# Optimization experiments

Hardware: AMD Instinct MI355X
Metric: run time of the kernel (lower is better)

## Reference

```python
import jax, jax.numpy as jnp
import numpy as np

NUM_GRAPHS = 256
N_NODES = 128          # nodes per graph (equal-size graphs)
DEG = 16               # average degree
NUM_EDGES = NUM_GRAPHS * N_NODES * DEG
NUM_HEADS = 8
SCALE = 10.0
INF_REPLACE = 1.0


def setup_inputs() -> dict:
    key = jax.random.key(0)
    k1, k2, k3 = jax.random.split(key, 3)
    # each graph owns a contiguous block of N_NODES global node ids
    eg = jnp.repeat(jnp.arange(NUM_GRAPHS, dtype=jnp.int32), N_NODES * DEG)
    src_loc = jax.random.randint(k1, (NUM_EDGES,), 0, N_NODES, dtype=jnp.int32)
    dst_loc = jax.random.randint(k2, (NUM_EDGES,), 0, N_NODES, dtype=jnp.int32)
    edge_index = jnp.stack([eg * N_NODES + src_loc, eg * N_NODES + dst_loc])  # [2, E]
    edge_weight = jax.random.uniform(k3, (NUM_EDGES,), minval=0.1, maxval=1.0)
    batch = jnp.repeat(jnp.arange(NUM_GRAPHS, dtype=jnp.int32), N_NODES)  # [N_total]
    return {
        'edge_index': edge_index,
        'edge_weight': edge_weight,
        'batch': batch,
        'num_graphs': NUM_GRAPHS,
        'max_num_nodes': N_NODES,
    }


def _shortest_path_bias(edge_index, edge_weight, batch, num_graphs, max_num_nodes):
    G, n = num_graphs, max_num_nodes
    inf = jnp.inf
    # per-graph node offsets (graphs occupy contiguous node-id blocks)
    counts = jnp.bincount(batch, length=G)
    offsets = jnp.concatenate([jnp.zeros((1,), counts.dtype), jnp.cumsum(counts)[:-1]])
    src, dst = edge_index[0], edge_index[1]
    eg = batch[src]                              # graph id of each edge
    u = src - offsets[eg]                        # local node ids
    v = dst - offsets[eg]
    # self-loops are skipped in the original (masked to +inf -> no-op under min)
    w = jnp.where(src == dst, inf, edge_weight)

    # init dense distance: inf off-diagonal, 0 on diagonal, edge weights scattered
    dist = jnp.full((G, n, n), inf, dtype=edge_weight.dtype)
    diag = jnp.arange(n)
    dist = dist.at[:, diag, diag].set(0.0)
    dist = dist.at[eg, u, v].min(w)

    # batched Floyd-Warshall: d[i,j] = min(d[i,j], d[i,k] + d[k,j]) for all graphs
    def body(d, k):
        col = jax.lax.dynamic_slice_in_dim(d, k, 1, axis=2)  # [G, n, 1] = d[:, :, k]
        row = jax.lax.dynamic_slice_in_dim(d, k, 1, axis=1)  # [G, 1, n] = d[:, k, :]
        return jnp.minimum(d, col + row), None
    dist, _ = jax.lax.scan(body, dist, jnp.arange(n))

    # replace unreachable with 2 * max finite distance (per graph)
    finite = jnp.isfinite(dist)
    fmax = jnp.max(jnp.where(finite, dist, -inf), axis=(1, 2), keepdims=True)
    unreach = jnp.where(jnp.isfinite(fmax), 2.0 * fmax, INF_REPLACE)
    dist = jnp.where(finite, dist, unreach)

    # normalize per graph and scale
    max_val = jnp.maximum(jnp.max(dist, axis=(1, 2), keepdims=True), 1e-8)
    bias = -SCALE * (dist / max_val)
    bias = jnp.nan_to_num(bias, nan=0.0, posinf=-1e6, neginf=-1e6)

    # expand over heads and flatten to [B*H, n, n]
    bias = jnp.broadcast_to(bias[:, None], (G, NUM_HEADS, n, n))
    return bias.reshape(G * NUM_HEADS, n, n)


def reference(edge_index, edge_weight, batch, num_graphs, max_num_nodes):
    return _shortest_path_bias(edge_index, edge_weight, batch, num_graphs, max_num_nodes)
```

## Files before the change

### kernel.cpp

```cpp
#include <hip/hip_runtime.h>

#define NHEADS 8
#define NN     128
#define NCELL  (NN * NN)
#define NT     512
#define SCALE_F 10.0f

typedef float nfloat4 __attribute__((ext_vector_type(4)));

#define RP_O 0
#define RP_N 2048
#define CP_As 4096
#define CP_Bs 6208
#define DPS  8320
#define RED  8640

template<int CBN>
__device__ __forceinline__ void extract_panels(const float (&dd)[4][8], float* lds,
                                               const int kbn, const int t,
                                               const int rgrp, const int cgrp,
                                               const int cpbase)
{
    if ((rgrp >> 2) == kbn) {
        const int q = rgrp & 3;
        #pragma unroll
        for (int rr = 0; rr < 4; ++rr) {
            const int iloc = 4 * q + rr;
            #pragma unroll
            for (int c = 0; c < 2; ++c) {
                *reinterpret_cast<float4*>(
                    &lds[RP_O + iloc * 128 + (cgrp << 2) + (c << 6)]) =
                    make_float4(dd[rr][c*4+0], dd[rr][c*4+1],
                                dd[rr][c*4+2], dd[rr][c*4+3]);
            }
        }
        const int p = cgrp - 4 * (kbn & 3);
        if ((unsigned)p < 4u) {
            #pragma unroll
            for (int rr = 0; rr < 4; ++rr) {
                *reinterpret_cast<float4*>(&lds[DPS + (4*q+rr) * 20 + (p << 2)]) =
                    make_float4(dd[rr][CBN+0], dd[rr][CBN+1],
                                dd[rr][CBN+2], dd[rr][CBN+3]);
            }
        }
    }
    {
        const int q2 = cgrp - 4 * (kbn & 3);
        if ((unsigned)q2 < 4u) {
            #pragma unroll
            for (int e = 0; e < 4; ++e) {
                const int m = 4 * q2 + e;
                *reinterpret_cast<float4*>(&lds[cpbase + m * 132 + (rgrp << 2)]) =
                    make_float4(dd[0][CBN+e], dd[1][CBN+e],
                                dd[2][CBN+e], dd[3][CBN+e]);
            }
        }
    }
}

__device__ __forceinline__ void closure(float* lds, const int t, const int kbn)
{
    if ((t >> 6) == kbn) {
        asm volatile("s_waitcnt lgkmcnt(0)" ::: "memory");
        const int l  = t & 63;
        const int i  = l & 15;
        const int jq = l >> 4;
        float4 v = *reinterpret_cast<const float4*>(&lds[DPS + i*20 + (jq << 2)]);
        float T0 = v.x, T1 = v.y, T2 = v.z, T3 = v.w;
        #pragma unroll
        for (int k = 0; k < 16; ++k) {
            const int ksrc = ((k >> 2) << 4) | i;
            float dik;
            switch (k & 3) {
                case 0: dik = __shfl(T0, ksrc); break;
                case 1: dik = __shfl(T1, ksrc); break;
                case 2: dik = __shfl(T2, ksrc); break;
                default: dik = __shfl(T3, ksrc); break;
            }
            const int rsrc = (jq << 4) | k;
            const float r0 = __shfl(T0, rsrc);
            const float r1 = __shfl(T1, rsrc);
            const float r2 = __shfl(T2, rsrc);
            const float r3 = __shfl(T3, rsrc);
            T0 = fminf(T0, dik + r0);
            T1 = fminf(T1, dik + r1);
            T2 = fminf(T2, dik + r2);
            T3 = fminf(T3, dik + r3);
        }
        *reinterpret_cast<float4*>(&lds[DPS + i*20 + (jq << 2)]) =
            make_float4(T0, T1, T2, T3);
    }
}

__device__ __forceinline__ void bprime(float* lds, const int t)
{
    const float INF = __builtin_huge_valf();
    const int r  = t >> 5;
    const int j4 = (t & 31) << 2;
    float da[16];
    #pragma unroll
    for (int q = 0; q < 4; ++q) {
        float4 d4 = *reinterpret_cast<const float4*>(&lds[DPS + r*20 + (q << 2)]);
        da[4*q+0]=d4.x; da[4*q+1]=d4.y; da[4*q+2]=d4.z; da[4*q+3]=d4.w;
    }
    float a0 = INF, a1 = INF, a2 = INF, a3 = INF;
    #pragma unroll
    for (int m = 0; m < 16; ++m) {
        float4 rv = *reinterpret_cast<const float4*>(&lds[RP_O + m*128 + j4]);
        a0 = fminf(a0, da[m] + rv.x);
        a1 = fminf(a1, da[m] + rv.y);
        a2 = fminf(a2, da[m] + rv.z);
        a3 = fminf(a3, da[m] + rv.w);
    }
    *reinterpret_cast<float4*>(&lds[RP_N + r*128 + j4]) =
        make_float4(a0, a1, a2, a3);
}

__device__ __forceinline__ void cphase(float (&dd)[4][8], float* lds,
                                       const int rgrp, const int cgrp,
                                       const int cpbase)
{
    #pragma unroll
    for (int mq = 0; mq < 4; ++mq) {
        float4 cp[4], ra[4], rb[4];
        #pragma unroll
        for (int e = 0; e < 4; ++e) {
            const int m = 4*mq + e;
            cp[e] = *reinterpret_cast<const float4*>(&lds[cpbase + m*132 + (rgrp<<2)]);
            ra[e] = *reinterpret_cast<const float4*>(&lds[RP_N + m*128 + (cgrp<<2)]);
            rb[e] = *reinterpret_cast<const float4*>(&lds[RP_N + m*128 + (cgrp<<2) + 64]);
        }
        #pragma unroll
        for (int e2 = 0; e2 < 2; ++e2) {
            const float c0[4]  = {cp[2*e2].x, cp[2*e2].y, cp[2*e2].z, cp[2*e2].w};
            const float c1[4]  = {cp[2*e2+1].x, cp[2*e2+1].y, cp[2*e2+1].z, cp[2*e2+1].w};
            const float ra0[4] = {ra[2*e2].x, ra[2*e2].y, ra[2*e2].z, ra[2*e2].w};
            const float ra1[4] = {ra[2*e2+1].x, ra[2*e2+1].y, ra[2*e2+1].z, ra[2*e2+1].w};
            const float rb0[4] = {rb[2*e2].x, rb[2*e2].y, rb[2*e2].z, rb[2*e2].w};
            const float rb1[4] = {rb[2*e2+1].x, rb[2*e2+1].y, rb[2*e2+1].z, rb[2*e2+1].w};
            #pragma unroll
            for (int rr = 0; rr < 4; ++rr) {
                #pragma unroll
                for (int e = 0; e < 4; ++e) {
                    dd[rr][e]   = fminf(fminf(dd[rr][e],   c0[rr] + ra0[e]), c1[rr] + ra1[e]);
                    dd[rr][4+e] = fminf(fminf(dd[rr][4+e], c0[rr] + rb0[e]), c1[rr] + rb1[e]);
                }
            }
        }
    }
}

__global__ __launch_bounds__(NT, 2)
void spb_fw_kernel(const int* __restrict__ edge_index,
                   const float* __restrict__ edge_weight,
                   const int num_edges, const int epg,
                   float* __restrict__ out)
{
    __shared__ float lds[NCELL];
    const float INF = __builtin_huge_valf();
    const int t    = threadIdx.x;
    const int g    = blockIdx.x;
    const int cgrp = t & 15;
    const int rgrp = t >> 4;

    const int ebase = g * epg;
    int esrc[4], edst[4]; float ew[4];
    #pragma unroll
    for (int k = 0; k < 4; ++k) {
        int e = t + k * NT;
        e = (e < epg) ? e : (epg - 1);
        const int idx = ebase + e;
        esrc[k] = edge_index[idx];
        edst[k] = edge_index[num_edges + idx];
        ew[k]   = edge_weight[idx];
    }

    #pragma unroll
    for (int c = 0; c < 8; ++c) {
        const int m   = t + (c << 9);
        const int i   = m >> 5;
        const int scm = m & 31;
        const int c0  = (scm ^ (i & 7)) << 2;
        float4 v;
        v.x = (c0 + 0 == i) ? 0.0f : INF;
        v.y = (c0 + 1 == i) ? 0.0f : INF;
        v.z = (c0 + 2 == i) ? 0.0f : INF;
        v.w = (c0 + 3 == i) ? 0.0f : INF;
        *reinterpret_cast<float4*>(&lds[m << 2]) = v;
    }
    __syncthreads();

    #pragma unroll
    for (int k = 0; k < 4; ++k) {
        const int u = esrc[k] - g * NN;
        const int v = edst[k] - g * NN;
        if (u != v && (unsigned)u < (unsigned)NN && (unsigned)v < (unsigned)NN) {
            const int a = (u << 7) + (v ^ ((u & 7) << 2));
            atomicMin(reinterpret_cast<int*>(&lds[a]), __float_as_int(ew[k]));
        }
    }
    __syncthreads();

    float dd[4][8];
    #pragma unroll
    for (int rr = 0; rr < 4; ++rr) {
        const int i = (rgrp << 2) + rr;
        const int s = i & 7;
        #pragma unroll
        for (int c = 0; c < 2; ++c) {
            float4 v = *reinterpret_cast<const float4*>(
                &lds[(i << 7) + (((cgrp + 16*c) ^ s) << 2)]);
            dd[rr][c*4+0]=v.x; dd[rr][c*4+1]=v.y; dd[rr][c*4+2]=v.z; dd[rr][c*4+3]=v.w;
        }
    }
    __syncthreads();

    extract_panels<0>(dd, lds, 0, t, rgrp, cgrp, CP_As);
    closure(lds, t, 0);
    __syncthreads();

    #pragma unroll 1
    for (int kb = 0; kb < 8; ++kb) {
        bprime(lds, t);
        __syncthreads();
        const int kbn = kb + 1;
        const bool shadow = (kb < 7) && ((t >> 6) == kbn);
        if (shadow) __builtin_amdgcn_s_setprio(1);
        cphase(dd, lds, rgrp, cgrp, (kb & 1) ? CP_Bs : CP_As);
        if (kb < 7) {
            const int cpb = (kbn & 1) ? CP_Bs : CP_As;
            if (kbn < 4) extract_panels<0>(dd, lds, kbn, t, rgrp, cgrp, cpb);
            else         extract_panels<4>(dd, lds, kbn, t, rgrp, cgrp, cpb);
            closure(lds, t, kbn);
        }
        if (shadow) __builtin_amdgcn_s_setprio(0);
        __syncthreads();
    }

    float mF = 0.0f, mA = 0.0f;
    #pragma unroll
    for (int rr = 0; rr < 4; ++rr)
        #pragma unroll
        for (int j = 0; j < 8; ++j) {
            const float v = dd[rr][j];
            mA = fmaxf(mA, v);
            mF = fmaxf(mF, v < INF ? v : 0.0f);
        }
    #pragma unroll
    for (int o = 32; o > 0; o >>= 1) {
        mF = fmaxf(mF, __shfl_xor(mF, o));
        mA = fmaxf(mA, __shfl_xor(mA, o));
    }
    if ((t & 63) == 0) {
        lds[RED + ((t >> 6) << 1)]     = mF;
        lds[RED + ((t >> 6) << 1) + 1] = mA;
    }
    __syncthreads();
    mF = lds[RED]; mA = lds[RED + 1];
    #pragma unroll
    for (int wv = 1; wv < 8; ++wv) {
        mF = fmaxf(mF, lds[RED + wv*2]);
        mA = fmaxf(mA, lds[RED + wv*2 + 1]);
    }
    const float twoF  = 2.0f * mF;
    const float maxv  = fmaxf((mA == INF) ? twoF : mF, 1e-8f);
    const float nscal = -SCALE_F / maxv;

    float* const outg = out + (size_t)g * (NHEADS * NCELL);
    #pragma unroll
    for (int rr = 0; rr < 4; ++rr) {
        const int i = (rgrp << 2) + rr;
        #pragma unroll
        for (int c = 0; c < 2; ++c) {
            nfloat4 v;
            v.x = ((dd[rr][c*4+0] == INF) ? twoF : dd[rr][c*4+0]) * nscal;
            v.y = ((dd[rr][c*4+1] == INF) ? twoF : dd[rr][c*4+1]) * nscal;
            v.z = ((dd[rr][c*4+2] == INF) ? twoF : dd[rr][c*4+2]) * nscal;
            v.w = ((dd[rr][c*4+3] == INF) ? twoF : dd[rr][c*4+3]) * nscal;
            const int o = (i << 7) + (cgrp << 2) + (c << 6);
            #pragma unroll
            for (int h = 0; h < NHEADS; ++h) {
                __builtin_nontemporal_store(
                    v, reinterpret_cast<nfloat4*>(&outg[h * NCELL + o]));
            }
        }
    }
}

extern "C" void kernel_launch(void* const* d_in, const int* in_sizes, int n_in,
                              void* d_out, int out_size, void* d_ws, size_t ws_size,
                              hipStream_t stream)
{
    const int*   edge_index  = (const int*)d_in[0];
    const float* edge_w      = (const float*)d_in[1];
    const int E    = in_sizes[1];
    const int Ntot = in_sizes[2];
    const int G    = Ntot / NN;
    const int epg  = E / G;
    float* out = (float*)d_out;
    spb_fw_kernel<<<G, NT, 0, stream>>>(edge_index, edge_w, E, epg, out);
}
```

Measured before the change: 61.25 us.

## Move row-panel update into owning wave and double-buffer it to drop a barrier

The block-wide bprime step, which needed its own __syncthreads before the C-phase, is replaced by a per-wave bprime_wave run by the wave that owns the next diagonal block, right after its closure. The new row panel goes into alternating LDS buffers (RP_NA/RP_NB), so it can be produced during the previous iteration's shadow work. This removes one block-wide barrier per k-block. The cost is that a single wave now does all of bprime, lengthening the critical path for that wave, and LDS use grows.

```diff
diff --git a/kernel.cpp b/kernel.cpp
--- a/kernel.cpp
+++ b/kernel.cpp
@@ -8,12 +8,13 @@
 
 typedef float nfloat4 __attribute__((ext_vector_type(4)));
 
-#define RP_O 0
-#define RP_N 2048
-#define CP_As 4096
-#define CP_Bs 6208
-#define DPS  8320
-#define RED  8640
+#define RP_O  0
+#define RP_NA 2048
+#define RP_NB 4096
+#define CP_As 6144
+#define CP_Bs 8256
+#define DPS   10368
+#define RED   10688
 
 template<int CBN>
 __device__ __forceinline__ void extract_panels(const float (&dd)[4][8], float* lds,
@@ -92,33 +93,46 @@
     }
 }
 
-__device__ __forceinline__ void bprime(float* lds, const int t)
-{
-    const float INF = __builtin_huge_valf();
-    const int r  = t >> 5;
-    const int j4 = (t & 31) << 2;
-    float da[16];
-    #pragma unroll
-    for (int q = 0; q < 4; ++q) {
-        float4 d4 = *reinterpret_cast<const float4*>(&lds[DPS + r*20 + (q << 2)]);
-        da[4*q+0]=d4.x; da[4*q+1]=d4.y; da[4*q+2]=d4.z; da[4*q+3]=d4.w;
-    }
-    float a0 = INF, a1 = INF, a2 = INF, a3 = INF;
-    #pragma unroll
-    for (int m = 0; m < 16; ++m) {
-        float4 rv = *reinterpret_cast<const float4*>(&lds[RP_O + m*128 + j4]);
-        a0 = fminf(a0, da[m] + rv.x);
-        a1 = fminf(a1, da[m] + rv.y);
-        a2 = fminf(a2, da[m] + rv.z);
-        a3 = fminf(a3, da[m] + rv.w);
-    }
-    *reinterpret_cast<float4*>(&lds[RP_N + r*128 + j4]) =
-        make_float4(a0, a1, a2, a3);
+__device__ __forceinline__ void bprime_wave(float* lds, const int t,
+                                            const int kbn, const int rpn)
+{
+    if ((t >> 6) == kbn) {
+        asm volatile("s_waitcnt lgkmcnt(0)" ::: "memory");
+        const float INF = __builtin_huge_valf();
+        const int l  = t & 63;
+        const int j4 = (l & 31) << 2;
+        const int rb = l >> 5;
+        float4 R[16];
+        #pragma unroll
+        for (int m = 0; m < 16; ++m)
+            R[m] = *reinterpret_cast<const float4*>(&lds[RP_O + m*128 + j4]);
+        #pragma unroll
+        for (int q = 0; q < 8; ++q) {
+            const int r = rb + (q << 1);
+            float4 d0 = *reinterpret_cast<const float4*>(&lds[DPS + r*20 + 0]);
+            float4 d1 = *reinterpret_cast<const float4*>(&lds[DPS + r*20 + 4]);
+            float4 d2 = *reinterpret_cast<const float4*>(&lds[DPS + r*20 + 8]);
+            float4 d3 = *reinterpret_cast<const float4*>(&lds[DPS + r*20 + 12]);
+            const float da[16] = {d0.x,d0.y,d0.z,d0.w, d1.x,d1.y,d1.z,d1.w,
+                                  d2.x,d2.y,d2.z,d2.w, d3.x,d3.y,d3.z,d3.w};
+            float a0 = INF, a1 = INF, a2 = INF, a3 = INF;
+            #pragma unroll
+            for (int mp = 0; mp < 8; ++mp) {
+                const int m0 = 2*mp, m1 = 2*mp + 1;
+                a0 = fminf(fminf(a0, da[m0] + R[m0].x), da[m1] + R[m1].x);
+                a1 = fminf(fminf(a1, da[m0] + R[m0].y), da[m1] + R[m1].y);
+                a2 = fminf(fminf(a2, da[m0] + R[m0].z), da[m1] + R[m1].z);
+                a3 = fminf(fminf(a3, da[m0] + R[m0].w), da[m1] + R[m1].w);
+            }
+            *reinterpret_cast<float4*>(&lds[rpn + r*128 + j4]) =
+                make_float4(a0, a1, a2, a3);
+        }
+    }
 }
 
 __device__ __forceinline__ void cphase(float (&dd)[4][8], float* lds,
                                        const int rgrp, const int cgrp,
-                                       const int cpbase)
+                                       const int cpbase, const int rpn)
 {
     #pragma unroll
     for (int mq = 0; mq < 4; ++mq) {
@@ -127,8 +141,8 @@
         for (int e = 0; e < 4; ++e) {
             const int m = 4*mq + e;
             cp[e] = *reinterpret_cast<const float4*>(&lds[cpbase + m*132 + (rgrp<<2)]);
-            ra[e] = *reinterpret_cast<const float4*>(&lds[RP_N + m*128 + (cgrp<<2)]);
-            rb[e] = *reinterpret_cast<const float4*>(&lds[RP_N + m*128 + (cgrp<<2) + 64]);
+            ra[e] = *reinterpret_cast<const float4*>(&lds[rpn + m*128 + (cgrp<<2)]);
+            rb[e] = *reinterpret_cast<const float4*>(&lds[rpn + m*128 + (cgrp<<2) + 64]);
         }
         #pragma unroll
         for (int e2 = 0; e2 < 2; ++e2) {
@@ -217,21 +231,24 @@
 
     extract_panels<0>(dd, lds, 0, t, rgrp, cgrp, CP_As);
     closure(lds, t, 0);
+    bprime_wave(lds, t, 0, RP_NA);
     __syncthreads();
 
     #pragma unroll 1
     for (int kb = 0; kb < 8; ++kb) {
-        bprime(lds, t);
-        __syncthreads();
         const int kbn = kb + 1;
         const bool shadow = (kb < 7) && ((t >> 6) == kbn);
         if (shadow) __builtin_amdgcn_s_setprio(1);
-        cphase(dd, lds, rgrp, cgrp, (kb & 1) ? CP_Bs : CP_As);
+        cphase(dd, lds, rgrp, cgrp,
+               (kb & 1) ? CP_Bs : CP_As,
+               (kb & 1) ? RP_NB : RP_NA);
         if (kb < 7) {
             const int cpb = (kbn & 1) ? CP_Bs : CP_As;
+            const int rpn = (kbn & 1) ? RP_NB : RP_NA;
             if (kbn < 4) extract_panels<0>(dd, lds, kbn, t, rgrp, cgrp, cpb);
             else         extract_panels<4>(dd, lds, kbn, t, rgrp, cgrp, cpb);
             closure(lds, t, kbn);
+            bprime_wave(lds, t, kbn, rpn);
         }
         if (shadow) __builtin_amdgcn_s_setprio(0);
         __syncthreads();
```

After: 70.66 us. 15.4% more time.
